# Optimization experiments

Hardware: AMD Instinct MI355X
Metric: run time of the kernel (lower is better)

The kernel has to match this reference:

```python
import jax, jax.numpy as jnp
import numpy as np

G = 32          # num graphs
NPG = 512       # nodes per graph
EPG = 4096      # edges per graph
DN = 128        # node/edge feat dim
DP = 64         # node identifier dim d_p
DE_ID = 64      # type identifier dim d_e
H = 768         # hidden_dim
IN_DIM = DN + 2 * DP + DE_ID  # 320


def setup_inputs() -> dict:
    key = jax.random.key(0)
    ks = jax.random.split(key, 9)
    N = G * NPG
    E = G * EPG
    x = jax.random.normal(ks[0], (N, DN), jnp.float32)
    edge_attr = jax.random.normal(ks[1], (E, DN), jnp.float32)
    P = jax.random.normal(ks[2], (N, DP), jnp.float32)  # ORF node identifiers
    E_V = jax.random.normal(ks[3], (1, DE_ID), jnp.float32) * 0.1
    E_E = jax.random.normal(ks[4], (1, DE_ID), jnp.float32) * 0.1
    W = jax.random.normal(ks[5], (H, IN_DIM), jnp.float32) / np.sqrt(IN_DIM)
    b = jnp.zeros((H,), jnp.float32)
    graph_token = jax.random.normal(ks[6], (1, H), jnp.float32) * 0.1
    # edges stay within their graph and are sorted by graph id
    base = jnp.repeat(jnp.arange(G, dtype=jnp.int32) * NPG, EPG)  # [E]
    src = base + jax.random.randint(ks[7], (E,), 0, NPG, jnp.int32)
    dst = base + jax.random.randint(ks[8], (E,), 0, NPG, jnp.int32)
    edge_index = jnp.stack([src, dst], axis=0)  # [2, E]
    batch = jnp.repeat(jnp.arange(G, dtype=jnp.int32), NPG)  # [N]
    return {
        "x": x, "edge_attr": edge_attr, "P": P,
        "E_V": E_V, "E_E": E_E, "W": W, "b": b, "graph_token": graph_token,
        "edge_index": edge_index, "batch": batch,
        "num_graphs": G, "max_node_num": NPG, "max_edge_num": EPG,
    }


def reference(x, edge_attr, P, E_V, E_E, W, b, graph_token,
              edge_index, batch, num_graphs, max_node_num, max_edge_num):
    N = x.shape[0]
    E = edge_index.shape[1]
    Hd = W.shape[0]
    d_e = E_V.shape[1]

    # node tokens: [x | P | P | E_V] @ W^T + b
    X_v = jnp.concatenate([x, P, P, jnp.broadcast_to(E_V, (N, d_e))], axis=1)
    X_v_proj = X_v @ W.T + b  # [N, H]

    # edge tokens: [edge_attr | P_u | P_v | E_E] @ W^T + b
    P_u = P[edge_index[0]]
    P_v = P[edge_index[1]]
    X_e = jnp.concatenate([edge_attr, P_u, P_v, jnp.broadcast_to(E_E, (E, d_e))], axis=1)
    X_e_proj = X_e @ W.T + b  # [E, H]

    # ragged -> padded packing (replaces per-graph python loop)
    ones_n = jnp.ones((N,), jnp.int32)
    node_num = jax.ops.segment_sum(ones_n, batch, num_segments=num_graphs)  # [G]
    node_ptr = jnp.cumsum(node_num) - node_num  # exclusive prefix sum
    node_pos = jnp.arange(N, dtype=jnp.int32) - node_ptr[batch]  # position within graph

    edge_batch = batch[edge_index[0]]  # [E]
    ones_e = jnp.ones((E,), jnp.int32)
    edge_num = jax.ops.segment_sum(ones_e, edge_batch, num_segments=num_graphs)
    edge_ptr = jnp.cumsum(edge_num) - edge_num
    edge_pos = jnp.arange(E, dtype=jnp.int32) - edge_ptr[edge_batch]

    seq_len = 1 + max_node_num + max_edge_num  # +1 for [graph] token
    tokens = jnp.zeros((num_graphs, seq_len, Hd), X_v_proj.dtype)
    tokens = tokens.at[:, 0, :].set(graph_token[0])
    tokens = tokens.at[batch, 1 + node_pos].set(X_v_proj)
    tokens = tokens.at[edge_batch, 1 + max_node_num + edge_pos].set(X_e_proj)

    attention_masks = jnp.zeros((num_graphs, seq_len), bool)
    attention_masks = attention_masks.at[:, 0].set(True)
    attention_masks = attention_masks.at[batch, 1 + node_pos].set(True)
    attention_masks = attention_masks.at[edge_batch, 1 + max_node_num + edge_pos].set(True)

    return tokens, attention_masks
```

## Files before the change

kernel.cpp:

```cpp
#include <hip/hip_runtime.h>
#include <stdint.h>

#define NG   32
#define NPG  512
#define EPG  4096
#define DN   128
#define DP   64
#define NN   (NG*NPG)
#define NE   (NG*EPG)
#define KD   320
#define HD   768
#define SEQ  (1+NPG+EPG)
#define TOK_ELEMS ((size_t)NG*SEQ*HD)
#define MASK_ELEMS ((size_t)NG*SEQ)

typedef unsigned short u16;
typedef __attribute__((ext_vector_type(8))) __bf16 bf16x8;
typedef __attribute__((ext_vector_type(8))) short  s16x8;
typedef __attribute__((ext_vector_type(4))) float  f32x4;

__device__ __forceinline__ u16 f2bf(float f) {
    uint32_t u = __builtin_bit_cast(uint32_t, f);
    u += 0x7fffu + ((u >> 16) & 1u);
    return (u16)(u >> 16);
}

__device__ __forceinline__ int b_off(int row, int kb) {
    return ((row >> 1) << 7) + ((row & 1) << 6) + (kb ^ (((row >> 1) & 3) << 4));
}

__global__ void ptr_k(const int* __restrict__ batch, const int* __restrict__ eidx,
                      int* __restrict__ nptr, int* __restrict__ eptr) {
    int t = threadIdx.x;
    if (t < NG) {
        int g = t, lo = 0, hi = NN;
        while (lo < hi) { int mid = (lo + hi) >> 1; if (batch[mid] < g) lo = mid + 1; else hi = mid; }
        nptr[g] = lo;
    } else if (t < 2 * NG) {
        int g = t - NG, lo = 0, hi = NE;
        while (lo < hi) { int mid = (lo + hi) >> 1; if (batch[eidx[mid]] < g) lo = mid + 1; else hi = mid; }
        eptr[g] = lo;
    }
}

__global__ void wconv_k(const float* __restrict__ W, u16* __restrict__ Wb) {
    int i = blockIdx.x * 256 + threadIdx.x;
    if (i < KD * HD) Wb[i] = f2bf(W[i]);
}

__global__ void aux_k(const float* __restrict__ gt, float* __restrict__ out) {
    size_t i = (size_t)blockIdx.x * 256 + threadIdx.x;
    if (i < (size_t)NG * HD) {
        int g = (int)(i / HD), c = (int)(i % HD);
        out[(size_t)g * SEQ * HD + c] = gt[c];
    } else {
        size_t m = i - (size_t)NG * HD;
        if (m < MASK_ELEMS) out[TOK_ELEMS + m] = 1.0f;
    }
}

__global__ __launch_bounds__(256, 2)
void gemm_scatter(const float* __restrict__ x,  const float* __restrict__ ea,
                  const float* __restrict__ P,  const float* __restrict__ EV,
                  const float* __restrict__ EEv,const float* __restrict__ bias,
                  const int* __restrict__ eidx, const int* __restrict__ batch,
                  const u16* __restrict__ Wb,   const int* __restrict__ nptr,
                  const int* __restrict__ eptr, float* __restrict__ out)
{
    __shared__ __align__(16) char b_lds[2][8192];
    __shared__ int info_src[128], info_pu[128], info_pv[128], info_orow[128];

    const int tid = threadIdx.x;
    const int r0  = blockIdx.x * 128;
    const bool isNode = (r0 < NN);
    const float* feat = isNode ? x  : ea;
    const float* idv  = isNode ? EV : EEv;

    if (tid < 128) {
        int r = r0 + tid;
        if (isNode) {
            int g = batch[r];
            info_src[tid] = r; info_pu[tid] = r; info_pv[tid] = r;
            info_orow[tid] = g * SEQ + 1 + (r - nptr[g]);
        } else {
            int e = r - NN;
            int s = eidx[e], d = eidx[NE + e];
            int g = batch[s];
            info_src[tid] = e; info_pu[tid] = s; info_pv[tid] = d;
            info_orow[tid] = g * SEQ + 1 + NPG + (e - eptr[g]);
        }
    }
    __syncthreads();

    const int lane = tid & 63;
    const int wid  = tid >> 6;
    const int lrow = lane & 15;
    const int lq   = lane >> 4;

    bf16x8 afr[2][10];
    int obase[2][4];
    #pragma unroll
    for (int rb = 0; rb < 2; ++rb) {
        const int arow = wid * 32 + rb * 16 + lrow;
        const int fsrc = info_src[arow];
        const int pu   = info_pu[arow];
        const int pv   = info_pv[arow];
        #pragma unroll
        for (int s = 0; s < 10; ++s) {
            const int kg = s * 32 + lq * 8;
            const float* sp;
            if      (s < 4) sp = feat + (size_t)fsrc * DN + kg;
            else if (s < 6) sp = P + (size_t)pu * DP + (kg - DN);
            else if (s < 8) sp = P + (size_t)pv * DP + (kg - DN - DP);
            else            sp = idv + (kg - DN - 2 * DP);
            f32x4 f0 = *reinterpret_cast<const f32x4*>(sp);
            f32x4 f1 = *reinterpret_cast<const f32x4*>(sp + 4);
            s16x8 v;
            v[0]=(short)f2bf(f0[0]); v[1]=(short)f2bf(f0[1]);
            v[2]=(short)f2bf(f0[2]); v[3]=(short)f2bf(f0[3]);
            v[4]=(short)f2bf(f1[0]); v[5]=(short)f2bf(f1[1]);
            v[6]=(short)f2bf(f1[2]); v[7]=(short)f2bf(f1[3]);
            afr[rb][s] = __builtin_bit_cast(bf16x8, v);
        }
        #pragma unroll
        for (int j = 0; j < 4; ++j)
            obase[rb][j] = info_orow[wid * 32 + rb * 16 + lq * 4 + j] * HD;
    }

    const int nl0 = tid >> 2;
    const int nl1 = nl0 + 64;
    const int kb  = (tid & 3) * 16;

    s16x8 pre0, pre1;
    {
        pre0 = *reinterpret_cast<const s16x8*>(Wb + (size_t)nl0 * KD + kb / 2);
        pre1 = *reinterpret_cast<const s16x8*>(Wb + (size_t)nl1 * KD + kb / 2);
    }

    for (int nt = 0; nt < 6; ++nt) {
        const int n0 = nt * 128;
        f32x4 acc[2][8];
        #pragma unroll
        for (int rb = 0; rb < 2; ++rb)
            #pragma unroll
            for (int i = 0; i < 8; ++i) acc[rb][i] = (f32x4)0.f;

        #pragma unroll
        for (int kt = 0; kt < 10; ++kt) {
            char* bb = b_lds[kt & 1];
            *reinterpret_cast<s16x8*>(bb + b_off(nl0, kb)) = pre0;
            *reinterpret_cast<s16x8*>(bb + b_off(nl1, kb)) = pre1;
            {
                int t  = nt * 10 + kt;
                int tn = (t < 59) ? t + 1 : 59;
                int ntn = tn / 10, ktn = tn - ntn * 10;
                const u16* q = Wb + (size_t)(ntn * 128) * KD + ktn * 32 + kb / 2;
                pre0 = *reinterpret_cast<const s16x8*>(q + (size_t)nl0 * KD);
                pre1 = *reinterpret_cast<const s16x8*>(q + (size_t)nl1 * KD);
            }
            asm volatile("s_waitcnt lgkmcnt(0)" ::: "memory");
            __builtin_amdgcn_sched_barrier(0);
            __builtin_amdgcn_s_barrier();
            #pragma unroll
            for (int ni = 0; ni < 8; ++ni) {
                bf16x8 bf = *reinterpret_cast<const bf16x8*>(
                    bb + b_off(ni * 16 + lrow, lq * 16));
                acc[0][ni] = __builtin_amdgcn_mfma_f32_16x16x32_bf16(afr[0][kt], bf, acc[0][ni], 0, 0, 0);
                acc[1][ni] = __builtin_amdgcn_mfma_f32_16x16x32_bf16(afr[1][kt], bf, acc[1][ni], 0, 0, 0);
            }
        }

        #pragma unroll
        for (int ni = 0; ni < 8; ++ni) {
            float bv = bias[n0 + ni * 16 + lrow];
            #pragma unroll
            for (int rb = 0; rb < 2; ++rb)
                #pragma unroll
                for (int j = 0; j < 4; ++j)
                    out[obase[rb][j] + n0 + ni * 16 + lrow] = acc[rb][ni][j] + bv;
        }
    }
}

extern "C" void kernel_launch(void* const* d_in, const int* in_sizes, int n_in,
                              void* d_out, int out_size, void* d_ws, size_t ws_size,
                              hipStream_t stream) {
    const float* x    = (const float*)d_in[0];
    const float* ea   = (const float*)d_in[1];
    const float* P    = (const float*)d_in[2];
    const float* EV   = (const float*)d_in[3];
    const float* EEv  = (const float*)d_in[4];
    const float* W    = (const float*)d_in[5];
    const float* bias = (const float*)d_in[6];
    const float* gt   = (const float*)d_in[7];
    const int* eidx   = (const int*)d_in[8];
    const int* batch  = (const int*)d_in[9];

    float* out = (float*)d_out;
    u16* Wb  = (u16*)d_ws;
    int* ints = (int*)((char*)d_ws + (size_t)KD * HD * 2);
    int *nptr = ints, *eptr = ints + 32;

    ptr_k<<<1, 64, 0, stream>>>(batch, eidx, nptr, eptr);
    wconv_k<<<(KD * HD + 255) / 256, 256, 0, stream>>>(W, Wb);
    aux_k<<<(int)(((size_t)NG * HD + MASK_ELEMS + 255) / 256), 256, 0, stream>>>(gt, out);
    gemm_scatter<<<dim3((NN + NE) / 128), 256, 0, stream>>>(
        x, ea, P, EV, EEv, bias, eidx, batch, Wb, nptr, eptr, out);
}
```

Measured before the change: 172.2 us.

## Stream W tiles into LDS via async global_load_lds with triple buffering

Replaces the register-staged double-buffered W tile loads with direct global-to-LDS async loads into a three-deep ring of 16KB buffers, each holding two k-steps. Prefetch runs two tiles ahead and only one barrier is needed per pair of k-steps, so global latency should hide better and fewer barriers and VGPRs are used. LDS use rises from 16KB to 48KB per block, which may cut occupancy below the two blocks per CU the launch bounds request. The hand-computed swizzled addresses and the vmcnt accounting also risk subtle ordering bugs.

```diff
diff --git a/kernel.cpp b/kernel.cpp
--- a/kernel.cpp
+++ b/kernel.cpp
@@ -67,10 +67,44 @@
                   const u16* __restrict__ Wb,   const int* __restrict__ nptr,
                   const int* __restrict__ eptr, float* __restrict__ out)
 {
-    __shared__ __align__(16) char b_lds[2][8192];
+    __shared__ __align__(16) char b_lds[3][16384];
     __shared__ int info_src[128], info_pu[128], info_pv[128], info_orow[128];
 
-    const int tid = threadIdx.x;
+    const int tid  = threadIdx.x;
+    const int lane = tid & 63;
+    const int wid  = tid >> 6;
+    const int lrow = lane & 15;
+    const int lq   = lane >> 4;
+
+    uint32_t lconst[4];
+    uint32_t ldsoff[4];
+    #pragma unroll
+    for (int i = 0; i < 4; ++i) {
+        uint32_t q   = (uint32_t)((wid * 4 + i) * 1024 + lane * 16);
+        uint32_t sub = q >> 13;
+        uint32_t qq  = q & 8191u;
+        uint32_t row = 2 * (qq >> 7) + ((qq >> 6) & 1);
+        uint32_t kb  = (qq & 0x30u) ^ (((qq >> 7) & 3u) << 4);
+        lconst[i] = row * (KD * 2) + sub * 64 + kb;
+        ldsoff[i] = (uint32_t)((wid * 4 + i) * 1024);
+    }
+    const char* WbB = (const char*)Wb;
+
+    auto issue_tile = [&](int p) {
+        const int nt = p / 5, kp = p - nt * 5;
+        const uint32_t base = (uint32_t)(nt * (128 * KD * 2) + kp * 128);
+        char* lb = &b_lds[p % 3][0];
+        #pragma unroll
+        for (int i = 0; i < 4; ++i) {
+            __builtin_amdgcn_global_load_lds(
+                (const uint32_t*)(WbB + base + lconst[i]),
+                (uint32_t*)(lb + ldsoff[i]), 16, 0, 0);
+        }
+    };
+
+    issue_tile(0);
+    issue_tile(1);
+
     const int r0  = blockIdx.x * 128;
     const bool isNode = (r0 < NN);
     const float* feat = isNode ? x  : ea;
@@ -91,11 +125,6 @@
         }
     }
     __syncthreads();
-
-    const int lane = tid & 63;
-    const int wid  = tid >> 6;
-    const int lrow = lane & 15;
-    const int lq   = lane >> 4;
 
     bf16x8 afr[2][10];
     int obase[2][4];
@@ -127,16 +156,9 @@
             obase[rb][j] = info_orow[wid * 32 + rb * 16 + lq * 4 + j] * HD;
     }
 
-    const int nl0 = tid >> 2;
-    const int nl1 = nl0 + 64;
-    const int kb  = (tid & 3) * 16;
-
-    s16x8 pre0, pre1;
-    {
-        pre0 = *reinterpret_cast<const s16x8*>(Wb + (size_t)nl0 * KD + kb / 2);
-        pre1 = *reinterpret_cast<const s16x8*>(Wb + (size_t)nl1 * KD + kb / 2);
-    }
-
+    const int roff = b_off(lrow, lq * 16);
+
+    int pglob = 0;
     for (int nt = 0; nt < 6; ++nt) {
         const int n0 = nt * 128;
         f32x4 acc[2][8];
@@ -146,27 +168,26 @@
             for (int i = 0; i < 8; ++i) acc[rb][i] = (f32x4)0.f;
 
         #pragma unroll
-        for (int kt = 0; kt < 10; ++kt) {
-            char* bb = b_lds[kt & 1];
-            *reinterpret_cast<s16x8*>(bb + b_off(nl0, kb)) = pre0;
-            *reinterpret_cast<s16x8*>(bb + b_off(nl1, kb)) = pre1;
-            {
-                int t  = nt * 10 + kt;
-                int tn = (t < 59) ? t + 1 : 59;
-                int ntn = tn / 10, ktn = tn - ntn * 10;
-                const u16* q = Wb + (size_t)(ntn * 128) * KD + ktn * 32 + kb / 2;
-                pre0 = *reinterpret_cast<const s16x8*>(q + (size_t)nl0 * KD);
-                pre1 = *reinterpret_cast<const s16x8*>(q + (size_t)nl1 * KD);
-            }
-            asm volatile("s_waitcnt lgkmcnt(0)" ::: "memory");
+        for (int kp = 0; kp < 5; ++kp, ++pglob) {
+            asm volatile("s_waitcnt vmcnt(4)" ::: "memory");
             __builtin_amdgcn_sched_barrier(0);
             __builtin_amdgcn_s_barrier();
+            __builtin_amdgcn_sched_barrier(0);
+            {
+                int pn = pglob + 2; if (pn > 29) pn = 29;
+                issue_tile(pn);
+            }
+            const char* bb = &b_lds[pglob % 3][0];
             #pragma unroll
-            for (int ni = 0; ni < 8; ++ni) {
-                bf16x8 bf = *reinterpret_cast<const bf16x8*>(
-                    bb + b_off(ni * 16 + lrow, lq * 16));
-                acc[0][ni] = __builtin_amdgcn_mfma_f32_16x16x32_bf16(afr[0][kt], bf, acc[0][ni], 0, 0, 0);
-                acc[1][ni] = __builtin_amdgcn_mfma_f32_16x16x32_bf16(afr[1][kt], bf, acc[1][ni], 0, 0, 0);
+            for (int kk = 0; kk < 2; ++kk) {
+                const int kt = kp * 2 + kk;
+                const char* bs = bb + kk * 8192;
+                #pragma unroll
+                for (int ni = 0; ni < 8; ++ni) {
+                    bf16x8 bf = *reinterpret_cast<const bf16x8*>(bs + ni * 1024 + roff);
+                    acc[0][ni] = __builtin_amdgcn_mfma_f32_16x16x32_bf16(afr[0][kt], bf, acc[0][ni], 0, 0, 0);
+                    acc[1][ni] = __builtin_amdgcn_mfma_f32_16x16x32_bf16(afr[1][kt], bf, acc[1][ni], 0, 0, 0);
+                }
             }
         }
 
```

Result: slower. 198.1 us (+15.0%).
